# Kernel tuning notes

Hardware: AMD Instinct MI355X
Metric: run time of the kernel (lower is better)

The kernel has to match this reference:

```python
import jax, jax.numpy as jnp
import numpy as np

SR = 48000
TIME_LENGTH = 62400  # int(1.3 * 48000)
MAX_VOICES = 16


def _conv1d_same(x, k, b):
    # x: [B, L, Cin], k: [K, Cin, Cout] -> [B, L, Cout], keras Conv1D padding='same'
    y = jax.lax.conv_general_dilated(x, k, (1,), 'SAME', dimension_numbers=('NWC', 'WIO', 'NWC'))
    return y + b


def setup_inputs() -> dict:
    key = jax.random.key(0)
    ks = jax.random.split(key, 20)
    B, L, D, C = 16, 250, 128, 32
    V = MAX_VOICES
    din = D + C
    w = lambda k, s: jax.random.normal(k, s, jnp.float32) * 0.05
    inp = {}
    inp['base_signal'] = jax.random.normal(ks[0], (B, TIME_LENGTH), jnp.float32)
    inp['z'] = jax.random.normal(ks[1], (B, L, D), jnp.float32)
    inp['cond'] = jax.random.uniform(ks[2], (B, C), jnp.float32)
    inp['fundamental_freq'] = jax.random.uniform(ks[3], (B,), jnp.float32)
    # param_predictor: Dense(256)->Dense(128)->Dense(64)->Dense(4)
    inp['W1'] = w(ks[4], (din, 256)); inp['b1'] = jnp.zeros((256,), jnp.float32)
    inp['W2'] = w(ks[5], (256, 128)); inp['b2'] = jnp.zeros((128,), jnp.float32)
    inp['W3'] = w(ks[6], (128, 64));  inp['b3'] = jnp.zeros((64,), jnp.float32)
    inp['W4'] = w(ks[7], (64, 4));    inp['b4'] = jnp.zeros((4,), jnp.float32)
    # voice_gain_net: Conv1D(128,7)->Conv1D(64,5)->Conv1D(V,3), input channels = D + C
    inp['K1'] = w(ks[8], (7, din, 128)); inp['cb1'] = jnp.zeros((128,), jnp.float32)
    inp['K2'] = w(ks[9], (5, 128, 64));  inp['cb2'] = jnp.zeros((64,), jnp.float32)
    inp['K3'] = w(ks[10], (3, 64, V));   inp['cb3'] = jnp.zeros((V,), jnp.float32)
    return inp


def reference(base_signal, z, cond, fundamental_freq,
              W1, b1, W2, b2, W3, b3, W4, b4,
              K1, cb1, K2, cb2, K3, cb3):
    B, T = base_signal.shape
    L = z.shape[1]
    V = MAX_VOICES
    # ---- global param predictor ----
    z_global = jnp.mean(z, axis=1)
    x = jnp.concatenate([z_global, cond], axis=-1)
    h = jax.nn.relu(x @ W1 + b1)
    h = jax.nn.relu(h @ W2 + b2)
    h = jax.nn.relu(h @ W3 + b3)
    params = h @ W4 + b4  # [B,4]
    num_voices = 1.0 + 14.0 * jax.nn.sigmoid(params[:, 0:1])  # [B,1]
    detune_cents = params[:, 1:2] * 50.0                       # [B,1] (unused downstream, as in source)
    spread = jax.nn.sigmoid(params[:, 2:3])                    # [B,1]
    depth = jax.nn.sigmoid(params[:, 3:4]) * 0.5               # [B,1]
    # ---- per-voice gain envelopes at latent rate ----
    z_cond = jnp.concatenate([z, jnp.broadcast_to(cond[:, None, :], (B, L, cond.shape[-1]))], axis=-1)
    g = jax.nn.relu(_conv1d_same(z_cond, K1, cb1))
    g = jax.nn.relu(_conv1d_same(g, K2, cb2))
    g = _conv1d_same(g, K3, cb3)  # [B, L, V]
    # TF bilinear resize (half-pixel centers) L -> T along time axis
    scale = L / T
    src = jnp.clip((jnp.arange(T, dtype=jnp.float32) + 0.5) * scale - 0.5, 0.0, L - 1.0)
    i0 = jnp.floor(src).astype(jnp.int32)
    i1 = jnp.minimum(i0 + 1, L - 1)
    frac = (src - i0.astype(jnp.float32))[None, :, None]
    vg = g[:, i0, :] * (1.0 - frac) + g[:, i1, :] * frac
    voice_gains = jax.nn.softplus(vg)  # [B, T, V]
    # ---- 16-voice detune/roll/LFO-modulate/accumulate, vectorized over voices ----
    pos = (np.arange(V) - (V - 1) / 2.0) / V            # static [V]
    shifts = np.trunc(pos * 20.0).astype(np.int64)      # int() truncation as in source
    gidx = (np.arange(T)[None, :] - shifts[:, None]) % T  # static [V, T] gather for tf.roll
    shifted = base_signal[:, jnp.asarray(gidx)]         # [B, V, T]
    t = jnp.arange(T, dtype=jnp.float32) / SR
    lfo_freq = 3.0 + 0.3 * jnp.arange(V, dtype=jnp.float32)
    lfo = jnp.sin(2.0 * np.pi * lfo_freq[:, None] * t[None, :])  # [V, T]
    modulated = shifted * (1.0 + 0.2 * depth[:, 0][:, None, None] * lfo[None])  # [B, V, T]
    pan = 1.0 - jnp.abs(jnp.asarray(pos, dtype=jnp.float32))[None, :] * spread * 0.5  # [B, V]
    unison = jnp.einsum('bvt,btv,bv->bt', modulated, voice_gains, pan)  # [B, T]
    # ---- soft voice-count mask and normalization ----
    voice_mask = jax.nn.sigmoid((num_voices - jnp.arange(V, dtype=jnp.float32)[None, :]) * 2.0)  # [B, V]
    norm = jnp.sqrt(jnp.sum(voice_mask, axis=-1, keepdims=True) + 1e-6)  # [B, 1]
    gain_sum = jnp.einsum('btv,bv->bt', voice_gains, voice_mask)  # [B, T]
    return gain_sum / (norm + 1e-6) * unison
```

## Files before the change

kernel.cpp:

```cpp
#include <hip/hip_runtime.h>
#include <hip/hip_bf16.h>
#include <math.h>

#define L_LEN 250
#define D_DIM 128
#define C_DIM 32
#define DIN   160
#define NV    16
#define T_LEN 62400
#define CB    244
#define XROWS 272
#define XR2   256
#define NXB   (16 * XROWS * 160)
#define NK1   (128 * 1120)
#define NK2   (64 * 640)
#define NPAD  (16 * 6 * 128)

typedef short short8 __attribute__((ext_vector_type(8)));
typedef float f32x4  __attribute__((ext_vector_type(4)));

__global__ __launch_bounds__(256) void prep_kernel(
        const float* __restrict__ z, const float* __restrict__ cond,
        const float* __restrict__ K1, const float* __restrict__ K2,
        __hip_bfloat16* __restrict__ Xb, __hip_bfloat16* __restrict__ K1t,
        __hip_bfloat16* __restrict__ K2t, __hip_bfloat16* __restrict__ g1b) {
    int idx = blockIdx.x * 256 + threadIdx.x;
    if (idx < NXB) {
        int b   = idx / (XROWS * 160);
        int rem = idx - b * (XROWS * 160);
        int r   = rem / 160;
        int ic  = rem - r * 160;
        int l   = r - 3;
        float v = 0.f;
        if (l >= 0 && l < L_LEN)
            v = (ic < D_DIM) ? z[((size_t)b * L_LEN + l) * D_DIM + ic]
                             : cond[b * C_DIM + (ic - D_DIM)];
        Xb[idx] = __float2bfloat16(v);
    } else if (idx < NXB + NK1) {
        int j  = idx - NXB;
        int oc = j / 1120;
        int k  = j - oc * 1120;
        K1t[j] = __float2bfloat16(K1[(size_t)k * 128 + oc]);
    } else if (idx < NXB + NK1 + NK2) {
        int j  = idx - NXB - NK1;
        int oc = j / 640;
        int k  = j - oc * 640;
        K2t[j] = __float2bfloat16(K2[(size_t)k * 64 + oc]);
    } else if (idx < NXB + NK1 + NK2 + NPAD) {
        int j  = idx - NXB - NK1 - NK2;
        int b  = j / (6 * 128);
        int rem = j - b * (6 * 128);
        int rr = rem >> 7;
        int ic = rem & 127;
        int r  = (rr < 2) ? rr : 250 + rr;
        g1b[((size_t)b * XR2 + r) * 128 + ic] = __float2bfloat16(0.f);
    }
}

__global__ __launch_bounds__(256) void conv1_mfma_mlp_kernel(
        const short* __restrict__ Xb, const short* __restrict__ K1t,
        const float* __restrict__ cb1, __hip_bfloat16* __restrict__ g1b,
        const float* __restrict__ z, const float* __restrict__ cond,
        const float* __restrict__ W1, const float* __restrict__ b1,
        const float* __restrict__ W2, const float* __restrict__ b2,
        const float* __restrict__ W3, const float* __restrict__ b3,
        const float* __restrict__ W4, const float* __restrict__ b4,
        float* __restrict__ P) {
    int tid = threadIdx.x;
    if (blockIdx.x < 16) {
        int b = blockIdx.x;
        __shared__ float buf[2176];
        float* xb = buf;
        float* h1 = buf + 160;
        float* h2 = buf + 416;
        float* h3 = buf + 544;
        float* pr = buf + 608;
        float* red = buf + 640;
        float4* sm4 = (float4*)(buf + 1152);
        {
            int c4 = tid & 31, rg = tid >> 5;
            const float4* zp = (const float4*)(z + (size_t)b * L_LEN * D_DIM) + c4;
            float4 acc = make_float4(0.f, 0.f, 0.f, 0.f);
            for (int r = rg; r < L_LEN; r += 8) {
                float4 v = zp[(size_t)r * 32];
                acc.x += v.x; acc.y += v.y; acc.z += v.z; acc.w += v.w;
            }
            sm4[rg * 32 + c4] = acc;
        }
        __syncthreads();
        if (tid < 32) {
            float4 acc = sm4[tid];
            #pragma unroll
            for (int g = 1; g < 8; ++g) {
                float4 v = sm4[g * 32 + tid];
                acc.x += v.x; acc.y += v.y; acc.z += v.z; acc.w += v.w;
            }
            const float inv = 1.0f / (float)L_LEN;
            acc.x *= inv; acc.y *= inv; acc.z *= inv; acc.w *= inv;
            ((float4*)xb)[tid] = acc;
        } else if (tid >= 128 && tid < DIN) {
            xb[tid] = cond[b * C_DIM + (tid - 128)];
        }
        __syncthreads();
        {
            const float* w = W1 + tid;
            float a0 = b1[tid], a1 = 0.f, a2 = 0.f, a3 = 0.f;
            float a4 = 0.f, a5 = 0.f, a6 = 0.f, a7 = 0.f;
            #pragma unroll 2
            for (int i = 0; i < DIN; i += 8) {
                a0 = fmaf(xb[i],     w[(size_t)(i)     * 256], a0);
                a1 = fmaf(xb[i + 1], w[(size_t)(i + 1) * 256], a1);
                a2 = fmaf(xb[i + 2], w[(size_t)(i + 2) * 256], a2);
                a3 = fmaf(xb[i + 3], w[(size_t)(i + 3) * 256], a3);
                a4 = fmaf(xb[i + 4], w[(size_t)(i + 4) * 256], a4);
                a5 = fmaf(xb[i + 5], w[(size_t)(i + 5) * 256], a5);
                a6 = fmaf(xb[i + 6], w[(size_t)(i + 6) * 256], a6);
                a7 = fmaf(xb[i + 7], w[(size_t)(i + 7) * 256], a7);
            }
            h1[tid] = fmaxf(((a0 + a1) + (a2 + a3)) + ((a4 + a5) + (a6 + a7)), 0.f);
        }
        __syncthreads();
        {
            int oc = tid & 127, hh = tid >> 7;
            const float* w = W2 + (size_t)(hh * 128) * 128 + oc;
            const float* x = h1 + hh * 128;
            float a0 = 0.f, a1 = 0.f, a2 = 0.f, a3 = 0.f;
            float a4 = 0.f, a5 = 0.f, a6 = 0.f, a7 = 0.f;
            #pragma unroll 2
            for (int i = 0; i < 128; i += 8) {
                a0 = fmaf(x[i],     w[(size_t)(i)     * 128], a0);
                a1 = fmaf(x[i + 1], w[(size_t)(i + 1) * 128], a1);
                a2 = fmaf(x[i + 2], w[(size_t)(i + 2) * 128], a2);
                a3 = fmaf(x[i + 3], w[(size_t)(i + 3) * 128], a3);
                a4 = fmaf(x[i + 4], w[(size_t)(i + 4) * 128], a4);
                a5 = fmaf(x[i + 5], w[(size_t)(i + 5) * 128], a5);
                a6 = fmaf(x[i + 6], w[(size_t)(i + 6) * 128], a6);
                a7 = fmaf(x[i + 7], w[(size_t)(i + 7) * 128], a7);
            }
            red[tid] = ((a0 + a1) + (a2 + a3)) + ((a4 + a5) + (a6 + a7));
        }
        __syncthreads();
        if (tid < 128) h2[tid] = fmaxf(red[tid] + red[tid + 128] + b2[tid], 0.f);
        __syncthreads();
        {
            int oc = tid & 63, qg = tid >> 6;
            const float* w = W3 + (size_t)(qg * 32) * 64 + oc;
            const float* x = h2 + qg * 32;
            float a0 = 0.f, a1 = 0.f, a2 = 0.f, a3 = 0.f;
            float a4 = 0.f, a5 = 0.f, a6 = 0.f, a7 = 0.f;
            #pragma unroll 2
            for (int i = 0; i < 32; i += 8) {
                a0 = fmaf(x[i],     w[(size_t)(i)     * 64], a0);
                a1 = fmaf(x[i + 1], w[(size_t)(i + 1) * 64], a1);
                a2 = fmaf(x[i + 2], w[(size_t)(i + 2) * 64], a2);
                a3 = fmaf(x[i + 3], w[(size_t)(i + 3) * 64], a3);
                a4 = fmaf(x[i + 4], w[(size_t)(i + 4) * 64], a4);
                a5 = fmaf(x[i + 5], w[(size_t)(i + 5) * 64], a5);
                a6 = fmaf(x[i + 6], w[(size_t)(i + 6) * 64], a6);
                a7 = fmaf(x[i + 7], w[(size_t)(i + 7) * 64], a7);
            }
            red[tid] = ((a0 + a1) + (a2 + a3)) + ((a4 + a5) + (a6 + a7));
        }
        __syncthreads();
        if (tid < 64)
            h3[tid] = fmaxf(red[tid] + red[tid + 64] + red[tid + 128] + red[tid + 192] + b3[tid], 0.f);
        __syncthreads();
        red[tid] = h3[tid >> 2] * W4[(tid >> 2) * 4 + (tid & 3)];
        __syncthreads();
        if (tid < 4) {
            float s = b4[tid];
            for (int k = 0; k < 64; ++k) s += red[k * 4 + tid];
            pr[tid] = s;
        }
        __syncthreads();
        if (tid == 0) {
            float num_voices = 1.0f + 14.0f / (1.0f + __expf(-pr[0]));
            float spread     = 1.0f / (1.0f + __expf(-pr[2]));
            float depth      = 0.5f / (1.0f + __expf(-pr[3]));
            float* Pb = P + b * 40;
            float msum = 0.f;
            for (int v = 0; v < NV; ++v) {
                float m = 1.0f / (1.0f + __expf(-(num_voices - (float)v) * 2.0f));
                msum += m;
                Pb[2 + v] = m;
                float pos = ((float)v - 7.5f) * (1.0f / 16.0f);
                Pb[2 + NV + v] = 1.0f - fabsf(pos) * spread * 0.5f;
            }
            float norm = sqrtf(msum + 1e-6f);
            Pb[0] = depth;
            Pb[1] = 1.0f / (norm + 1e-6f);
        }
        return;
    }
    int blk = blockIdx.x - 16;
    int b   = blk >> 4;
    int lt  = blk & 15;
    int l0  = lt * 16;
    int lane = tid & 63;
    int oc0g = (tid >> 6) * 32;
    int m  = lane & 15;
    int kg = lane >> 4;

    const short* Ab = Xb + ((size_t)(b * XROWS + l0 + m) * 160 + kg * 8);
    const short* Bb = K1t + ((size_t)(oc0g + m) * 1120 + kg * 8);

    f32x4 acc0 = {0.f, 0.f, 0.f, 0.f};
    f32x4 acc1 = {0.f, 0.f, 0.f, 0.f};
    #pragma unroll 1
    for (int tap = 0; tap < 7; ++tap) {
        const short* ap = Ab + tap * 160;
        const short* bp = Bb + tap * 160;
        #pragma unroll
        for (int ks = 0; ks < 5; ++ks) {
            short8 av  = *(const short8*)(ap + ks * 32);
            short8 bv0 = *(const short8*)(bp + ks * 32);
            short8 bv1 = *(const short8*)(bp + 16 * 1120 + ks * 32);
            acc0 = __builtin_amdgcn_mfma_f32_16x16x32_bf16(av, bv0, acc0, 0, 0, 0);
            acc1 = __builtin_amdgcn_mfma_f32_16x16x32_bf16(av, bv1, acc1, 0, 0, 0);
        }
    }
    float bias0 = cb1[oc0g + m];
    float bias1 = cb1[oc0g + m + 16];
    int rbase = l0 + kg * 4;
    #pragma unroll
    for (int j = 0; j < 4; ++j) {
        int lr = rbase + j;
        if (lr < L_LEN) {
            __hip_bfloat16* gp = g1b + ((size_t)(b * XR2) + lr + 2) * 128 + oc0g + m;
            gp[0]  = __float2bfloat16(fmaxf(acc0[j] + bias0, 0.f));
            gp[16] = __float2bfloat16(fmaxf(acc1[j] + bias1, 0.f));
        }
    }
}

__global__ __launch_bounds__(256) void conv2_mfma_kernel(
        const short* __restrict__ g1b, const short* __restrict__ K2t,
        float* __restrict__ g2) {
    int tid = threadIdx.x;
    int b   = blockIdx.x >> 4;
    int lt  = blockIdx.x & 15;
    int l0  = lt * 16;
    int lane = tid & 63;
    int oc0w = (tid >> 6) * 16;
    int m  = lane & 15;
    int kg = lane >> 4;

    const short* Ab = g1b + ((size_t)(b * XR2 + l0 + m) * 128 + kg * 8);
    const short* Bb = K2t + ((size_t)(oc0w + m) * 640 + kg * 8);

    f32x4 acc = {0.f, 0.f, 0.f, 0.f};
    #pragma unroll 1
    for (int tap = 0; tap < 5; ++tap) {
        const short* ap = Ab + tap * 128;
        const short* bp = Bb + tap * 128;
        #pragma unroll
        for (int ks = 0; ks < 4; ++ks) {
            short8 av = *(const short8*)(ap + ks * 32);
            short8 bv = *(const short8*)(bp + ks * 32);
            acc = __builtin_amdgcn_mfma_f32_16x16x32_bf16(av, bv, acc, 0, 0, 0);
        }
    }
    int rbase = l0 + kg * 4;
    #pragma unroll
    for (int j = 0; j < 4; ++j) {
        int l = rbase + j;
        if (l < L_LEN)
            g2[((size_t)b * L_LEN + l) * 64 + oc0w + m] = acc[j];
    }
}

__global__ __launch_bounds__(256) void conv3_main_kernel(
        const float* __restrict__ base, const float* __restrict__ g2,
        const float* __restrict__ cb2,
        const float* __restrict__ K3, const float* __restrict__ cb3,
        const float* __restrict__ P, float* __restrict__ out) {
    int b = blockIdx.x / CB;
    int c = blockIdx.x % CB;
    int t0 = c * 256;
    int tid = threadIdx.x;
    const float scale = 250.0f / 62400.0f;

    __shared__ float k3t[16][196];
    __shared__ float sA[6][68];
    __shared__ float g3loc[4][17];
    __shared__ float Pb[34];
    __shared__ float sbase[276];

    float src0 = ((float)t0 + 0.5f) * scale - 0.5f;
    src0 = fminf(fmaxf(src0, 0.0f), 249.0f);
    int L0 = (int)floorf(src0);

    const float* bs = base + (size_t)b * T_LEN;
    if (tid < 34) Pb[tid] = P[b * 40 + tid];
    for (int idx = tid; idx < 274; idx += 256) {
        int tt = t0 - 9 + idx;
        if (tt < 0) tt += T_LEN; else if (tt >= T_LEN) tt -= T_LEN;
        sbase[idx] = bs[tt];
    }
    for (int idx = tid; idx < 3 * 64 * 16; idx += 256) {
        int v  = idx & 15;
        int ti = idx >> 4;
        k3t[v][ti] = K3[ti * 16 + v];
    }
    for (int idx = tid; idx < 6 * 64; idx += 256) {
        int pl = idx >> 6;
        int i  = idx & 63;
        int p  = L0 - 1 + pl;
        float v = 0.f;
        if (p >= 0 && p < L_LEN)
            v = fmaxf(cb2[i] + g2[((size_t)b * L_LEN + p) * 64 + i], 0.f);
        sA[pl][i] = v;
    }
    __syncthreads();

    {
        int seg = tid & 3;
        int v   = (tid >> 2) & 15;
        int r   = tid >> 6;
        float acc = 0.f;
        #pragma unroll
        for (int tap = 0; tap < 3; ++tap) {
            const float* gr = &sA[r + tap][seg * 16];
            const float* kr = &k3t[v][tap * 64 + seg * 16];
            #pragma unroll
            for (int j = 0; j < 4; ++j) {
                float4 g = *(const float4*)&gr[j * 4];
                float4 k = *(const float4*)&kr[j * 4];
                acc = fmaf(g.x, k.x, acc);
                acc = fmaf(g.y, k.y, acc);
                acc = fmaf(g.z, k.z, acc);
                acc = fmaf(g.w, k.w, acc);
            }
        }
        acc += __shfl_xor(acc, 1);
        acc += __shfl_xor(acc, 2);
        if (seg == 0) g3loc[r][v] = acc + cb3[v];
    }
    __syncthreads();

    int t = t0 + tid;
    if (t >= T_LEN) return;
    float depth = Pb[0];
    float coef  = Pb[1];
    float src = ((float)t + 0.5f) * scale - 0.5f;
    src = fminf(fmaxf(src, 0.0f), 249.0f);
    float fi0 = floorf(src);
    int i0 = (int)fi0;
    int i1 = min(i0 + 1, L_LEN - 1);
    float frac = src - fi0;
    int r0 = i0 - L0;
    int r1 = i1 - L0;
    float vg[16];
    #pragma unroll
    for (int v = 0; v < NV; ++v) {
        float a = g3loc[r0][v];
        float d = g3loc[r1][v];
        vg[v] = fmaf(d - a, frac, a);
    }
    float tsec = (float)t * (1.0f / 48000.0f);
    const int shifts[NV] = {-9,-8,-6,-5,-4,-3,-1,0,0,1,3,4,5,6,8,9};
    float gain_sum = 0.f, uni = 0.f;
    #pragma unroll
    for (int v = 0; v < NV; ++v) {
        float x = vg[v];
        float sp = fmaxf(x, 0.f) + __logf(1.0f + __expf(-fabsf(x)));
        float fv = 3.0f + 0.3f * (float)v;
        float ph = fv * tsec;
        ph -= floorf(ph);
        float lfo = __builtin_amdgcn_sinf(ph);
        float mod = sbase[tid + 9 - shifts[v]] * fmaf(0.2f * depth, lfo, 1.0f);
        gain_sum = fmaf(sp, Pb[2 + v], gain_sum);
        uni      = fmaf(mod * sp, Pb[2 + NV + v], uni);
    }
    out[(size_t)b * T_LEN + t] = gain_sum * coef * uni;
}

__global__ void params_kernel(const float* __restrict__ z, const float* __restrict__ cond,
                              const float* __restrict__ W1, const float* __restrict__ b1,
                              const float* __restrict__ W2, const float* __restrict__ b2,
                              const float* __restrict__ W3, const float* __restrict__ b3,
                              const float* __restrict__ W4, const float* __restrict__ b4,
                              float* __restrict__ P) {
    int b = blockIdx.x;
    int tid = threadIdx.x;
    __shared__ float xb[DIN];
    __shared__ float zp2[128];
    __shared__ float h1[256];
    __shared__ float h2[128];
    __shared__ float h3[64];
    __shared__ float pr[4];
    {
        int i = tid & 127, half = tid >> 7;
        const float* zp = z + (size_t)b * L_LEN * D_DIM + i;
        float s = 0.f;
        for (int l = half; l < L_LEN; l += 2) s += zp[(size_t)l * D_DIM];
        if (half) zp2[i] = s;
        __syncthreads();
        if (!half) xb[i] = (s + zp2[i]) * (1.0f / (float)L_LEN);
        if (tid >= 128 && tid < DIN) xb[tid] = cond[b * C_DIM + (tid - 128)];
    }
    __syncthreads();
    {
        float acc = b1[tid];
        for (int i = 0; i < DIN; ++i) acc = fmaf(xb[i], W1[i * 256 + tid], acc);
        h1[tid] = fmaxf(acc, 0.f);
    }
    __syncthreads();
    if (tid < 128) {
        float acc = b2[tid];
        for (int i = 0; i < 256; ++i) acc = fmaf(h1[i], W2[i * 128 + tid], acc);
        h2[tid] = fmaxf(acc, 0.f);
    }
    __syncthreads();
    if (tid < 64) {
        float acc = b3[tid];
        for (int i = 0; i < 128; ++i) acc = fmaf(h2[i], W3[i * 64 + tid], acc);
        h3[tid] = fmaxf(acc, 0.f);
    }
    __syncthreads();
    if (tid < 4) {
        float acc = b4[tid];
        for (int i = 0; i < 64; ++i) acc = fmaf(h3[i], W4[i * 4 + tid], acc);
        pr[tid] = acc;
    }
    __syncthreads();
    if (tid == 0) {
        float num_voices = 1.0f + 14.0f / (1.0f + __expf(-pr[0]));
        float spread     = 1.0f / (1.0f + __expf(-pr[2]));
        float depth      = 0.5f / (1.0f + __expf(-pr[3]));
        float* Pb = P + b * 40;
        float msum = 0.f;
        for (int v = 0; v < NV; ++v) {
            float m = 1.0f / (1.0f + __expf(-(num_voices - (float)v) * 2.0f));
            msum += m;
            Pb[2 + v] = m;
            float pos = ((float)v - 7.5f) * (1.0f / 16.0f);
            Pb[2 + NV + v] = 1.0f - fabsf(pos) * spread * 0.5f;
        }
        float norm = sqrtf(msum + 1e-6f);
        Pb[0] = depth;
        Pb[1] = 1.0f / (norm + 1e-6f);
    }
}

__global__ void conv1_mono_kernel(const float* __restrict__ z, const float* __restrict__ cond,
                                  const float* __restrict__ K1, const float* __restrict__ cb1,
                                  float* __restrict__ g1) {
    int b  = blockIdx.x >> 4;
    int lt = blockIdx.x & 15;
    int l0 = lt * 16;
    int tid = threadIdx.x;
    __shared__ float sm[DIN][22];
    for (int idx = tid; idx < 22 * DIN; idx += 256) {
        int pl = idx / DIN;
        int i  = idx - pl * DIN;
        int p  = l0 - 3 + pl;
        float v = 0.f;
        if (p >= 0 && p < L_LEN)
            v = (i < D_DIM) ? z[((size_t)b * L_LEN + p) * D_DIM + i]
                            : cond[b * C_DIM + (i - D_DIM)];
        sm[i][pl] = v;
    }
    __syncthreads();
    int oc = tid & 127;
    int lb = (tid >> 7) * 8;
    float bias = cb1[oc];
    float acc[8];
    #pragma unroll
    for (int j = 0; j < 8; ++j) acc[j] = bias;
    for (int i = 0; i < DIN; ++i) {
        float zr[14];
        #pragma unroll
        for (int q = 0; q < 14; ++q) zr[q] = sm[i][lb + q];
        #pragma unroll
        for (int tap = 0; tap < 7; ++tap) {
            float k = K1[(size_t)(tap * DIN + i) * 128 + oc];
            #pragma unroll
            for (int j = 0; j < 8; ++j) acc[j] = fmaf(zr[tap + j], k, acc[j]);
        }
    }
    #pragma unroll
    for (int j = 0; j < 8; ++j) {
        int l = l0 + lb + j;
        if (l < L_LEN) g1[((size_t)b * L_LEN + l) * 128 + oc] = fmaxf(acc[j], 0.f);
    }
}

__global__ void conv2_mono_kernel(const float* __restrict__ g1,
                                  const float* __restrict__ K2, const float* __restrict__ cb2,
                                  float* __restrict__ g2) {
    int b  = blockIdx.x >> 4;
    int lt = blockIdx.x & 15;
    int l0 = lt * 16;
    int tid = threadIdx.x;
    __shared__ float sm[128][20];
    for (int idx = tid; idx < 20 * 128; idx += 256) {
        int pl = idx >> 7;
        int i  = idx & 127;
        int p  = l0 - 2 + pl;
        float v = (p >= 0 && p < L_LEN) ? g1[((size_t)b * L_LEN + p) * 128 + i] : 0.f;
        sm[i][pl] = v;
    }
    __syncthreads();
    int oc = tid & 63;
    int lb = (tid >> 6) * 4;
    float bias = cb2[oc];
    float acc[4];
    #pragma unroll
    for (int j = 0; j < 4; ++j) acc[j] = bias;
    for (int i = 0; i < 128; ++i) {
        float zr[8];
        #pragma unroll
        for (int q = 0; q < 8; ++q) zr[q] = sm[i][lb + q];
        #pragma unroll
        for (int tap = 0; tap < 5; ++tap) {
            float k = K2[(size_t)(tap * 128 + i) * 64 + oc];
            #pragma unroll
            for (int j = 0; j < 4; ++j) acc[j] = fmaf(zr[tap + j], k, acc[j]);
        }
    }
    #pragma unroll
    for (int j = 0; j < 4; ++j) {
        int l = l0 + lb + j;
        if (l < L_LEN) g2[((size_t)b * L_LEN + l) * 64 + oc] = fmaxf(acc[j], 0.f);
    }
}

__global__ void conv3_mono_kernel(const float* __restrict__ g2,
                                  const float* __restrict__ K3, const float* __restrict__ cb3,
                                  float* __restrict__ g3) {
    int b  = blockIdx.x >> 4;
    int lt = blockIdx.x & 15;
    int l0 = lt * 16;
    int tid = threadIdx.x;
    int v  = tid & 15;
    int ll = tid >> 4;
    int l  = l0 + ll;
    if (l >= L_LEN) return;
    float acc = cb3[v];
    #pragma unroll
    for (int tap = 0; tap < 3; ++tap) {
        int p = l + tap - 1;
        if (p < 0 || p >= L_LEN) continue;
        const float* gp = g2 + ((size_t)b * L_LEN + p) * 64;
        #pragma unroll
        for (int i = 0; i < 64; ++i) acc = fmaf(gp[i], K3[(size_t)(tap * 64 + i) * 16 + v], acc);
    }
    g3[((size_t)b * L_LEN + l) * 16 + v] = acc;
}

__global__ __launch_bounds__(256) void main_mono_kernel(
        const float* __restrict__ base, const float* __restrict__ g3,
        const float* __restrict__ P, float* __restrict__ out) {
    int b = blockIdx.x / CB;
    int c = blockIdx.x % CB;
    int t = c * 256 + threadIdx.x;
    __shared__ float Pb[34];
    if (threadIdx.x < 34) Pb[threadIdx.x] = P[b * 40 + threadIdx.x];
    __syncthreads();
    if (t >= T_LEN) return;
    float depth = Pb[0];
    float coef  = Pb[1];
    const float scale = 250.0f / 62400.0f;
    float src = ((float)t + 0.5f) * scale - 0.5f;
    src = fminf(fmaxf(src, 0.0f), 249.0f);
    float fi0 = floorf(src);
    int i0 = (int)fi0;
    int i1 = min(i0 + 1, L_LEN - 1);
    float frac = src - fi0;
    const float4* r0 = (const float4*)(g3 + ((size_t)b * L_LEN + i0) * NV);
    const float4* r1 = (const float4*)(g3 + ((size_t)b * L_LEN + i1) * NV);
    float vg[16];
    #pragma unroll
    for (int q = 0; q < 4; ++q) {
        float4 a = r0[q];
        float4 d = r1[q];
        vg[q * 4 + 0] = fmaf(d.x - a.x, frac, a.x);
        vg[q * 4 + 1] = fmaf(d.y - a.y, frac, a.y);
        vg[q * 4 + 2] = fmaf(d.z - a.z, frac, a.z);
        vg[q * 4 + 3] = fmaf(d.w - a.w, frac, a.w);
    }
    float tsec = (float)t * (1.0f / 48000.0f);
    const float* bs = base + (size_t)b * T_LEN;
    const int shifts[NV] = {-9,-8,-6,-5,-4,-3,-1,0,0,1,3,4,5,6,8,9};
    float gain_sum = 0.f, uni = 0.f;
    #pragma unroll
    for (int v = 0; v < NV; ++v) {
        float x = vg[v];
        float sp = fmaxf(x, 0.f) + __logf(1.0f + __expf(-fabsf(x)));
        float fv = 3.0f + 0.3f * (float)v;
        float ph = fv * tsec;
        ph -= floorf(ph);
        float lfo = __builtin_amdgcn_sinf(ph);
        int tb = t - shifts[v];
        if (tb < 0) tb += T_LEN; else if (tb >= T_LEN) tb -= T_LEN;
        float mod = bs[tb] * fmaf(0.2f * depth, lfo, 1.0f);
        gain_sum = fmaf(sp, Pb[2 + v], gain_sum);
        uni      = fmaf(mod * sp, Pb[2 + NV + v], uni);
    }
    out[(size_t)b * T_LEN + t] = gain_sum * coef * uni;
}

extern "C" void kernel_launch(void* const* d_in, const int* in_sizes, int n_in,
                              void* d_out, int out_size, void* d_ws, size_t ws_size,
                              hipStream_t stream) {
    const float* base = (const float*)d_in[0];
    const float* z    = (const float*)d_in[1];
    const float* cond = (const float*)d_in[2];
    const float* W1 = (const float*)d_in[4];  const float* b1 = (const float*)d_in[5];
    const float* W2 = (const float*)d_in[6];  const float* b2 = (const float*)d_in[7];
    const float* W3 = (const float*)d_in[8];  const float* b3 = (const float*)d_in[9];
    const float* W4 = (const float*)d_in[10]; const float* b4 = (const float*)d_in[11];
    const float* K1 = (const float*)d_in[12]; const float* cb1 = (const float*)d_in[13];
    const float* K2 = (const float*)d_in[14]; const float* cb2 = (const float*)d_in[15];
    const float* K3 = (const float*)d_in[16]; const float* cb3 = (const float*)d_in[17];
    float* out = (float*)d_out;

    int B = in_sizes[0] / T_LEN;

    float* ws = (float*)d_ws;
    const size_t XBF  = NXB / 2;
    const size_t K1F  = NK1 / 2;
    const size_t K2F  = NK2 / 2;
    const size_t G1BF = (size_t)16 * XR2 * 128 / 2;
    const size_t G2   = (size_t)16 * L_LEN * 64;
    size_t need = (1024 + XBF + K1F + K2F + G1BF + G2) * sizeof(float);

    float* P = ws;
    if (ws_size >= need) {
        __hip_bfloat16* Xb  = (__hip_bfloat16*)(ws + 1024);
        __hip_bfloat16* K1t = (__hip_bfloat16*)(ws + 1024 + XBF);
        __hip_bfloat16* K2t = (__hip_bfloat16*)(ws + 1024 + XBF + K1F);
        __hip_bfloat16* g1b = (__hip_bfloat16*)(ws + 1024 + XBF + K1F + K2F);
        float* g2 = ws + 1024 + XBF + K1F + K2F + G1BF;

        int prep_blocks = (NXB + NK1 + NK2 + NPAD + 255) / 256;
        prep_kernel<<<prep_blocks, 256, 0, stream>>>(z, cond, K1, K2, Xb, K1t, K2t, g1b);
        conv1_mfma_mlp_kernel<<<16 + 256, 256, 0, stream>>>(
            (const short*)Xb, (const short*)K1t, cb1, g1b, z, cond,
            W1, b1, W2, b2, W3, b3, W4, b4, P);
        conv2_mfma_kernel<<<256, 256, 0, stream>>>(
            (const short*)g1b, (const short*)K2t, g2);
        conv3_main_kernel<<<B * CB, 256, 0, stream>>>(base, g2, cb2, K3, cb3, P, out);
    } else {
        float* g1 = ws + 1024;
        float* g2 = g1 + (size_t)B * L_LEN * 128;
        float* g3 = g2 + (size_t)B * L_LEN * 64;
        params_kernel<<<B, 256, 0, stream>>>(z, cond, W1, b1, W2, b2, W3, b3, W4, b4, P);
        conv1_mono_kernel<<<B * 16, 256, 0, stream>>>(z, cond, K1, cb1, g1);
        conv2_mono_kernel<<<B * 16, 256, 0, stream>>>(g1, K2, cb2, g2);
        conv3_mono_kernel<<<B * 16, 256, 0, stream>>>(g2, K3, cb3, g3);
        main_mono_kernel<<<B * CB, 256, 0, stream>>>(base, g3, P, out);
    }
}
```

Measured before the change: 58.18 us.

## Fuse conv1 and conv2 into one kernel with halo recompute in shared memory

Merges the conv1 and conv2 kernels so each block computes a 24-row conv1 tile (16 rows plus a 4-row halo on each side) into shared memory as bf16, then runs conv2 from shared memory. This removes one kernel launch, the global g1 intermediate and the pad-zeroing work in the prep kernel. In exchange, conv1 work grows by about 50% because of the halo recompute, and a block-wide sync is added.

Result: no change. 57.74 us (-0.7%).

```diff
diff --git a/kernel.cpp b/kernel.cpp
--- a/kernel.cpp
+++ b/kernel.cpp
@@ -10,11 +10,9 @@
 #define T_LEN 62400
 #define CB    244
 #define XROWS 272
-#define XR2   256
 #define NXB   (16 * XROWS * 160)
 #define NK1   (128 * 1120)
 #define NK2   (64 * 640)
-#define NPAD  (16 * 6 * 128)
 
 typedef short short8 __attribute__((ext_vector_type(8)));
 typedef float f32x4  __attribute__((ext_vector_type(4)));
@@ -23,7 +21,7 @@
         const float* __restrict__ z, const float* __restrict__ cond,
         const float* __restrict__ K1, const float* __restrict__ K2,
         __hip_bfloat16* __restrict__ Xb, __hip_bfloat16* __restrict__ K1t,
-        __hip_bfloat16* __restrict__ K2t, __hip_bfloat16* __restrict__ g1b) {
+        __hip_bfloat16* __restrict__ K2t) {
     int idx = blockIdx.x * 256 + threadIdx.x;
     if (idx < NXB) {
         int b   = idx / (XROWS * 160);
@@ -46,20 +44,13 @@
         int oc = j / 640;
         int k  = j - oc * 640;
         K2t[j] = __float2bfloat16(K2[(size_t)k * 64 + oc]);
-    } else if (idx < NXB + NK1 + NK2 + NPAD) {
-        int j  = idx - NXB - NK1 - NK2;
-        int b  = j / (6 * 128);
-        int rem = j - b * (6 * 128);
-        int rr = rem >> 7;
-        int ic = rem & 127;
-        int r  = (rr < 2) ? rr : 250 + rr;
-        g1b[((size_t)b * XR2 + r) * 128 + ic] = __float2bfloat16(0.f);
-    }
-}
-
-__global__ __launch_bounds__(256) void conv1_mfma_mlp_kernel(
+    }
+}
+
+__global__ __launch_bounds__(256) void conv12_mlp_kernel(
         const short* __restrict__ Xb, const short* __restrict__ K1t,
-        const float* __restrict__ cb1, __hip_bfloat16* __restrict__ g1b,
+        const short* __restrict__ K2t,
+        const float* __restrict__ cb1, float* __restrict__ g2,
         const float* __restrict__ z, const float* __restrict__ cond,
         const float* __restrict__ W1, const float* __restrict__ b1,
         const float* __restrict__ W2, const float* __restrict__ b2,
@@ -67,6 +58,7 @@
         const float* __restrict__ W4, const float* __restrict__ b4,
         float* __restrict__ P) {
     int tid = threadIdx.x;
+    __shared__ __hip_bfloat16 g1loc[24][132];
     if (blockIdx.x < 16) {
         int b = blockIdx.x;
         __shared__ float buf[2176];
@@ -197,75 +189,71 @@
     int lt  = blk & 15;
     int l0  = lt * 16;
     int lane = tid & 63;
-    int oc0g = (tid >> 6) * 32;
+    int w    = tid >> 6;
     int m  = lane & 15;
     int kg = lane >> 4;
-
-    const short* Ab = Xb + ((size_t)(b * XROWS + l0 + m) * 160 + kg * 8);
-    const short* Bb = K1t + ((size_t)(oc0g + m) * 1120 + kg * 8);
-
-    f32x4 acc0 = {0.f, 0.f, 0.f, 0.f};
-    f32x4 acc1 = {0.f, 0.f, 0.f, 0.f};
+    int oc0g = w * 32;
+
     #pragma unroll 1
-    for (int tap = 0; tap < 7; ++tap) {
-        const short* ap = Ab + tap * 160;
-        const short* bp = Bb + tap * 160;
-        #pragma unroll
-        for (int ks = 0; ks < 5; ++ks) {
-            short8 av  = *(const short8*)(ap + ks * 32);
-            short8 bv0 = *(const short8*)(bp + ks * 32);
-            short8 bv1 = *(const short8*)(bp + 16 * 1120 + ks * 32);
-            acc0 = __builtin_amdgcn_mfma_f32_16x16x32_bf16(av, bv0, acc0, 0, 0, 0);
-            acc1 = __builtin_amdgcn_mfma_f32_16x16x32_bf16(av, bv1, acc1, 0, 0, 0);
-        }
-    }
-    float bias0 = cb1[oc0g + m];
-    float bias1 = cb1[oc0g + m + 16];
-    int rbase = l0 + kg * 4;
-    #pragma unroll
-    for (int j = 0; j < 4; ++j) {
-        int lr = rbase + j;
-        if (lr < L_LEN) {
-            __hip_bfloat16* gp = g1b + ((size_t)(b * XR2) + lr + 2) * 128 + oc0g + m;
-            gp[0]  = __float2bfloat16(fmaxf(acc0[j] + bias0, 0.f));
-            gp[16] = __float2bfloat16(fmaxf(acc1[j] + bias1, 0.f));
-        }
-    }
-}
-
-__global__ __launch_bounds__(256) void conv2_mfma_kernel(
-        const short* __restrict__ g1b, const short* __restrict__ K2t,
-        float* __restrict__ g2) {
-    int tid = threadIdx.x;
-    int b   = blockIdx.x >> 4;
-    int lt  = blockIdx.x & 15;
-    int l0  = lt * 16;
-    int lane = tid & 63;
-    int oc0w = (tid >> 6) * 16;
-    int m  = lane & 15;
-    int kg = lane >> 4;
-
-    const short* Ab = g1b + ((size_t)(b * XR2 + l0 + m) * 128 + kg * 8);
-    const short* Bb = K2t + ((size_t)(oc0w + m) * 640 + kg * 8);
-
-    f32x4 acc = {0.f, 0.f, 0.f, 0.f};
-    #pragma unroll 1
-    for (int tap = 0; tap < 5; ++tap) {
-        const short* ap = Ab + tap * 128;
-        const short* bp = Bb + tap * 128;
-        #pragma unroll
-        for (int ks = 0; ks < 4; ++ks) {
-            short8 av = *(const short8*)(ap + ks * 32);
-            short8 bv = *(const short8*)(bp + ks * 32);
-            acc = __builtin_amdgcn_mfma_f32_16x16x32_bf16(av, bv, acc, 0, 0, 0);
-        }
-    }
-    int rbase = l0 + kg * 4;
-    #pragma unroll
-    for (int j = 0; j < 4; ++j) {
-        int l = rbase + j;
-        if (l < L_LEN)
-            g2[((size_t)b * L_LEN + l) * 64 + oc0w + m] = acc[j];
+    for (int t0r = 0; t0r < 2; ++t0r) {
+        int lbase = l0 - 4 + t0r * 16;
+        f32x4 acc0 = {0.f, 0.f, 0.f, 0.f};
+        f32x4 acc1 = {0.f, 0.f, 0.f, 0.f};
+        const short* Bb = K1t + ((size_t)(oc0g + m) * 1120 + kg * 8);
+        #pragma unroll 1
+        for (int tap = 0; tap < 7; ++tap) {
+            int r = lbase + m + tap;
+            r = min(max(r, 0), XROWS - 1);
+            const short* ap = Xb + ((size_t)(b * XROWS + r) * 160 + kg * 8);
+            const short* bp = Bb + tap * 160;
+            #pragma unroll
+            for (int ks = 0; ks < 5; ++ks) {
+                short8 av  = *(const short8*)(ap + ks * 32);
+                short8 bv0 = *(const short8*)(bp + ks * 32);
+                short8 bv1 = *(const short8*)(bp + 16 * 1120 + ks * 32);
+                acc0 = __builtin_amdgcn_mfma_f32_16x16x32_bf16(av, bv0, acc0, 0, 0, 0);
+                acc1 = __builtin_amdgcn_mfma_f32_16x16x32_bf16(av, bv1, acc1, 0, 0, 0);
+            }
+        }
+        float bias0 = cb1[oc0g + m];
+        float bias1 = cb1[oc0g + m + 16];
+        #pragma unroll
+        for (int j = 0; j < 4; ++j) {
+            int l    = lbase + kg * 4 + j;
+            int lidx = t0r * 16 + kg * 4 + j;
+            if (lidx < 24) {
+                bool valid = (l >= 0 && l < L_LEN);
+                float v0 = valid ? fmaxf(acc0[j] + bias0, 0.f) : 0.f;
+                float v1 = valid ? fmaxf(acc1[j] + bias1, 0.f) : 0.f;
+                g1loc[lidx][oc0g + m]      = __float2bfloat16(v0);
+                g1loc[lidx][oc0g + m + 16] = __float2bfloat16(v1);
+            }
+        }
+    }
+    __syncthreads();
+
+    {
+        int oc2 = w * 16 + m;
+        const short* Bb2 = K2t + ((size_t)oc2 * 640 + kg * 8);
+        f32x4 acc = {0.f, 0.f, 0.f, 0.f};
+        #pragma unroll 1
+        for (int tap = 0; tap < 5; ++tap) {
+            const __hip_bfloat16* arow = &g1loc[m + 2 + tap][kg * 8];
+            const short* bp = Bb2 + tap * 128;
+            #pragma unroll
+            for (int ks = 0; ks < 4; ++ks) {
+                short8 av = *(const short8*)(arow + ks * 32);
+                short8 bv = *(const short8*)(bp + ks * 32);
+                acc = __builtin_amdgcn_mfma_f32_16x16x32_bf16(av, bv, acc, 0, 0, 0);
+            }
+        }
+        int rbase = l0 + kg * 4;
+        #pragma unroll
+        for (int j = 0; j < 4; ++j) {
+            int l = rbase + j;
+            if (l < L_LEN)
+                g2[((size_t)b * L_LEN + l) * 64 + oc2] = acc[j];
+        }
     }
 }
 
@@ -619,28 +607,24 @@
     int B = in_sizes[0] / T_LEN;
 
     float* ws = (float*)d_ws;
-    const size_t XBF  = NXB / 2;
-    const size_t K1F  = NK1 / 2;
-    const size_t K2F  = NK2 / 2;
-    const size_t G1BF = (size_t)16 * XR2 * 128 / 2;
-    const size_t G2   = (size_t)16 * L_LEN * 64;
-    size_t need = (1024 + XBF + K1F + K2F + G1BF + G2) * sizeof(float);
+    const size_t XBF = NXB / 2;
+    const size_t K1F = NK1 / 2;
+    const size_t K2F = NK2 / 2;
+    const size_t G2  = (size_t)16 * L_LEN * 64;
+    size_t need = (1024 + XBF + K1F + K2F + G2) * sizeof(float);
 
     float* P = ws;
     if (ws_size >= need) {
         __hip_bfloat16* Xb  = (__hip_bfloat16*)(ws + 1024);
         __hip_bfloat16* K1t = (__hip_bfloat16*)(ws + 1024 + XBF);
         __hip_bfloat16* K2t = (__hip_bfloat16*)(ws + 1024 + XBF + K1F);
-        __hip_bfloat16* g1b = (__hip_bfloat16*)(ws + 1024 + XBF + K1F + K2F);
-        float* g2 = ws + 1024 + XBF + K1F + K2F + G1BF;
-
-        int prep_blocks = (NXB + NK1 + NK2 + NPAD + 255) / 256;
-        prep_kernel<<<prep_blocks, 256, 0, stream>>>(z, cond, K1, K2, Xb, K1t, K2t, g1b);
-        conv1_mfma_mlp_kernel<<<16 + 256, 256, 0, stream>>>(
-            (const short*)Xb, (const short*)K1t, cb1, g1b, z, cond,
-            W1, b1, W2, b2, W3, b3, W4, b4, P);
-        conv2_mfma_kernel<<<256, 256, 0, stream>>>(
-            (const short*)g1b, (const short*)K2t, g2);
+        float* g2 = ws + 1024 + XBF + K1F + K2F;
+
+        int prep_blocks = (NXB + NK1 + NK2 + 255) / 256;
+        prep_kernel<<<prep_blocks, 256, 0, stream>>>(z, cond, K1, K2, Xb, K1t, K2t);
+        conv12_mlp_kernel<<<16 + 256, 256, 0, stream>>>(
+            (const short*)Xb, (const short*)K1t, (const short*)K2t,
+            cb1, g2, z, cond, W1, b1, W2, b2, W3, b3, W4, b4, P);
         conv3_main_kernel<<<B * CB, 256, 0, stream>>>(base, g2, cb2, K3, cb3, P, out);
     } else {
         float* g1 = ws + 1024;
```
